# Kernel optimization log

Measured on AMD Instinct MI355X. Metric: run time of the kernel, lower is better.

## Reference

```python
import jax, jax.numpy as jnp
import numpy as np

EMBED_DIM = 1024
NUM_HEADS = 8
HEAD_DIM = EMBED_DIM // NUM_HEADS


def setup_inputs() -> dict:
    key = jax.random.key(0)
    k1, k2, k3, k4, k5 = jax.random.split(key, 5)
    B, N, D = 4, 2048, EMBED_DIM
    scale = 1.0 / np.sqrt(D)
    return {
        "representation": jax.random.normal(k1, (B, N, D), dtype=jnp.float32),
        "W_qkv": jax.random.normal(k2, (D, 3 * D), dtype=jnp.float32) * scale,
        "b_qkv": jnp.zeros((3 * D,), dtype=jnp.float32),
        "W_proj": jax.random.normal(k3, (D, D), dtype=jnp.float32) * scale,
        "b_proj": jnp.zeros((D,), dtype=jnp.float32),
    }


def reference(representation, W_qkv, b_qkv, W_proj, b_proj):
    B, N, D = representation.shape
    H, Hd = NUM_HEADS, HEAD_DIM
    qkv = jnp.einsum("bnd,de->bne", representation, W_qkv) + b_qkv  # [B,N,3D]
    q, k, v = jnp.split(qkv, 3, axis=-1)
    # [B,N,D] -> [B,H,N,Hd]
    split_heads = lambda x: x.reshape(B, N, H, Hd).transpose(0, 2, 1, 3)
    q, k, v = split_heads(q), split_heads(k), split_heads(v)
    dots = jnp.einsum("bhqd,bhkd->bhqk", q, k) * (Hd ** -0.5)  # [B,H,N,N]
    attn = jax.nn.softmax(dots, axis=-1)
    out = jnp.einsum("bhqk,bhkd->bhqd", attn, v)
    out = out.transpose(0, 2, 1, 3).reshape(B, N, D)  # merge heads
    return jnp.einsum("bnd,de->bne", out, W_proj) + b_proj
```

## Files before the change

### kernel.cpp

```cpp
#include <hip/hip_runtime.h>
#include <hip/hip_bf16.h>
#include <cstdint>

typedef unsigned short u16;
typedef __attribute__((ext_vector_type(8))) short short8;
typedef __attribute__((ext_vector_type(4))) float f32x4;
typedef __attribute__((ext_vector_type(4))) unsigned short u16x4;
typedef __attribute__((ext_vector_type(4))) unsigned int u32x4;

#define NSEQ 2048
#define DMODEL 1024
#define NH 8
#define HD 128
#define KDIM 1024
#define QSCALE (0.08838834764831845f * 1.4426950408889634f)

__device__ __forceinline__ u16 f2b(float f) {
  __hip_bfloat16 h = __float2bfloat16(f);
  union { __hip_bfloat16 h; u16 u; } cv; cv.h = h; return cv.u;
}
__device__ __forceinline__ f32x4 zero4() { f32x4 z = {0.f, 0.f, 0.f, 0.f}; return z; }

__device__ __forceinline__ void gload_lds16(const u16* g, u16* l) {
  __builtin_amdgcn_global_load_lds(
      (__attribute__((address_space(1))) void*)g,
      (__attribute__((address_space(3))) void*)l, 16, 0, 0);
}

__device__ __forceinline__ int LK(int r) {
  return (r & 0x23) | ((r & 0x0C) << 1) | ((r & 0x10) >> 2);
}

__global__ void cvt_f32_bf16(const float* __restrict__ in, u16* __restrict__ out) {
  const size_t i = ((size_t)blockIdx.x * 256 + threadIdx.x) * 8;
  f32x4 a = *(const f32x4*)&in[i];
  f32x4 b = *(const f32x4*)&in[i + 4];
  short8 o;
#pragma unroll
  for (int j = 0; j < 4; ++j) { o[j] = (short)f2b(a[j]); o[4 + j] = (short)f2b(b[j]); }
  *(short8*)&out[i] = o;
}

__global__ void transpose_k(const float* __restrict__ in, u16* __restrict__ out,
                            int R, int C) {
  __shared__ u16 tile[32][33];
  const int tx = threadIdx.x, ty = threadIdx.y;
  const int c = blockIdx.x * 32 + tx;
  const int r0 = blockIdx.y * 32;
  for (int i = ty; i < 32; i += 8) tile[i][tx] = f2b(in[(size_t)(r0 + i) * C + c]);
  __syncthreads();
  const int oc = r0 + tx;
  const int c0 = blockIdx.x * 32;
  for (int i = ty; i < 32; i += 8) out[(size_t)(c0 + i) * R + oc] = tile[tx][i];
}

template <int MODE>
__global__ __launch_bounds__(256, 3) void gemm128(
    const u16* __restrict__ A, const u16* __restrict__ Bt,
    const float* __restrict__ bias, u16* __restrict__ o0,
    u16* __restrict__ o1, u16* __restrict__ o2, float* __restrict__ of) {
  __shared__ __align__(16) u16 sA[128 * 64];
  __shared__ __align__(16) u16 sB[128 * 64];

  const int tid = threadIdx.x;
  const int lane = tid & 63;
  const int w = tid >> 6;
  const int quad = lane >> 4, ln = lane & 15;
  const int m0 = blockIdx.y * 128, n0 = blockIdx.x * 128;
  const int wm = (w >> 1) * 64, wn = (w & 1) * 64;

  f32x4 acc[4][4];
#pragma unroll
  for (int i = 0; i < 4; ++i)
#pragma unroll
    for (int j = 0; j < 4; ++j) acc[i][j] = zero4();

  const int cbase = w * 4;
  for (int kb = 0; kb < KDIM / 64; ++kb) {
    __syncthreads();
    const int k0 = kb * 64;
#pragma unroll
    for (int i = 0; i < 4; ++i) {
      int c = (cbase + i) * 64 + lane;
      int r = c >> 3, s = c & 7;
      gload_lds16(A + (size_t)(m0 + r) * KDIM + k0 + s * 8, &sA[(cbase + i) * 512]);
      gload_lds16(Bt + (size_t)(n0 + r) * KDIM + k0 + s * 8, &sB[(cbase + i) * 512]);
    }
    __syncthreads();
#pragma unroll
    for (int ks = 0; ks < 2; ++ks) {
      short8 af[4], bf[4];
      const int kc = ks * 4 + quad;
#pragma unroll
      for (int t = 0; t < 4; ++t) {
        af[t] = *(const short8*)&sA[(wm + t * 16 + ln) * 64 + kc * 8];
        bf[t] = *(const short8*)&sB[(wn + t * 16 + ln) * 64 + kc * 8];
      }
#pragma unroll
      for (int mt = 0; mt < 4; ++mt)
#pragma unroll
        for (int nt = 0; nt < 4; ++nt)
          acc[mt][nt] = __builtin_amdgcn_mfma_f32_16x16x32_bf16(
              af[mt], bf[nt], acc[mt][nt], 0, 0, 0);
    }
  }

  if (MODE == 0) {
    const int which = n0 >> 10;
    const int h = (n0 & 1023) >> 7;
#pragma unroll
    for (int mt = 0; mt < 4; ++mt) {
      const int rbase = m0 + wm + mt * 16 + quad * 4;
      const int b = rbase >> 11;
      const int n = rbase & 2047;
#pragma unroll
      for (int nt = 0; nt < 4; ++nt) {
        const int dcol = wn + nt * 16 + ln;
        const float bv = bias[n0 + dcol];
        if (which == 0) {
          u16* p = o0 + ((size_t)(b * NH + h) * NSEQ + n) * HD + dcol;
#pragma unroll
          for (int rr = 0; rr < 4; ++rr)
            p[(size_t)rr * HD] = f2b((acc[mt][nt][rr] + bv) * QSCALE);
        } else if (which == 1) {
          u16* p = o1 + ((size_t)(b * NH + h) * NSEQ + n) * HD + dcol;
#pragma unroll
          for (int rr = 0; rr < 4; ++rr)
            p[(size_t)rr * HD] = f2b(acc[mt][nt][rr] + bv);
        } else {
          u16x4 pk;
#pragma unroll
          for (int rr = 0; rr < 4; ++rr) pk[rr] = f2b(acc[mt][nt][rr] + bv);
          *(u16x4*)&o2[((size_t)(b * NH + h) * HD + dcol) * NSEQ + n] = pk;
        }
      }
    }
  } else {
#pragma unroll
    for (int mt = 0; mt < 4; ++mt) {
      const int rbase = m0 + wm + mt * 16 + quad * 4;
#pragma unroll
      for (int nt = 0; nt < 4; ++nt) {
        const int col = n0 + wn + nt * 16 + ln;
        const float bv = bias[col];
#pragma unroll
        for (int rr = 0; rr < 4; ++rr)
          of[(size_t)(rbase + rr) * DMODEL + col] = acc[mt][nt][rr] + bv;
      }
    }
  }
}

__global__ __launch_bounds__(256, 2) void attn_fused(
    const u16* __restrict__ Q, const u16* __restrict__ K,
    const u16* __restrict__ Vt, u16* __restrict__ AO) {
  __shared__ __align__(16) u16 sK[2][64 * 128];
  __shared__ __align__(16) u16 sV[2][128 * 64];

  const int tid = threadIdx.x;
  const int w = tid >> 6, lane = tid & 63;
  const int quad = lane >> 4, ln = lane & 15;
  const int bh = blockIdx.y;
  const int q0 = blockIdx.x * 128;

  const u16* Qb = Q + ((size_t)bh * NSEQ + q0) * HD;
  const u16* Kb = K + (size_t)bh * NSEQ * HD;
  const u16* Vb = Vt + (size_t)bh * HD * NSEQ;

  int gk_off[4], gv_off[4];
#pragma unroll
  for (int j = 0; j < 4; ++j) {
    const int c = (w * 4 + j) * 64 + lane;
    const int rk = c >> 4, sk_ = c & 15;
    gk_off[j] = LK(rk) * HD + (sk_ ^ (rk & 7)) * 8;
    const int rv = c >> 3, sv_ = c & 7;
    gv_off[j] = rv * NSEQ + (sv_ ^ (rv & 7)) * 8;
  }

  int kfo[4][4], vfo[2][8];
#pragma unroll
  for (int n = 0; n < 4; ++n)
#pragma unroll
    for (int ks = 0; ks < 4; ++ks)
      kfo[n][ks] = (n * 16 + ln) * 128 + ((((ks << 2) | quad) ^ (ln & 7)) * 8);
#pragma unroll
  for (int ks2 = 0; ks2 < 2; ++ks2)
#pragma unroll
    for (int dt = 0; dt < 8; ++dt)
      vfo[ks2][dt] = (dt * 16 + ln) * 64 + ((((ks2 << 2) | quad) ^ (ln & 7)) * 8);

  short8 qf[2][4];
#pragma unroll
  for (int mt = 0; mt < 2; ++mt)
#pragma unroll
    for (int ks = 0; ks < 4; ++ks)
      qf[mt][ks] = *(const short8*)&Qb[(size_t)(w * 32 + mt * 16 + ln) * HD +
                                       ks * 32 + quad * 8];

  f32x4 o[2][8];
#pragma unroll
  for (int mt = 0; mt < 2; ++mt)
#pragma unroll
    for (int dt = 0; dt < 8; ++dt) o[mt][dt] = zero4();
  float l_part[2] = {0.f, 0.f};

#pragma unroll
  for (int j = 0; j < 4; ++j) {
    gload_lds16(Kb + gk_off[j], &sK[0][(w * 4 + j) * 512]);
    gload_lds16(Vb + gv_off[j], &sV[0][(w * 4 + j) * 512]);
  }

  union PU { u32x4 u; short8 s; };

#pragma unroll 1
  for (int it = 0; it < NSEQ / 128; ++it) {
#pragma unroll
    for (int c2 = 0; c2 < 2; ++c2) {
      __syncthreads();

      const int kvn = it * 128 + c2 * 64 + 64;
      if (kvn < NSEQ) {
#pragma unroll
        for (int j = 0; j < 4; ++j) {
          gload_lds16(Kb + (size_t)kvn * HD + gk_off[j],
                      &sK[c2 ^ 1][(w * 4 + j) * 512]);
          gload_lds16(Vb + kvn + gv_off[j], &sV[c2 ^ 1][(w * 4 + j) * 512]);
        }
      }
      const u16* skr = &sK[c2][0];
      const u16* svr = &sV[c2][0];

      __builtin_amdgcn_s_setprio(1);

      f32x4 sacc[4][2];
      PU ph[2][2];

      auto SM = [&](int m) {
#pragma unroll
        for (int mt = 0; mt < 2; ++mt) {
          float e0 = exp2f(sacc[m][mt][0]);
          float e1 = exp2f(sacc[m][mt][1]);
          float e2 = exp2f(sacc[m][mt][2]);
          float e3 = exp2f(sacc[m][mt][3]);
          l_part[mt] += (e0 + e1) + (e2 + e3);
          unsigned a0 = __float_as_uint(e0) + 0x8000u;
          unsigned a1 = __float_as_uint(e1) + 0x8000u;
          unsigned a2 = __float_as_uint(e2) + 0x8000u;
          unsigned a3 = __float_as_uint(e3) + 0x8000u;
          ph[mt][m >> 1].u[(m & 1) * 2 + 0] = __builtin_amdgcn_perm(a1, a0, 0x07060302);
          ph[mt][m >> 1].u[(m & 1) * 2 + 1] = __builtin_amdgcn_perm(a3, a2, 0x07060302);
        }
      };

#pragma unroll
      for (int n = 0; n < 4; ++n) {
#pragma unroll
        for (int mt = 0; mt < 2; ++mt) sacc[n][mt] = zero4();
#pragma unroll
        for (int ks = 0; ks < 4; ++ks) {
          short8 kf = *(const short8*)&skr[kfo[n][ks]];
          sacc[n][0] = __builtin_amdgcn_mfma_f32_16x16x32_bf16(
              kf, qf[0][ks], sacc[n][0], 0, 0, 0);
          sacc[n][1] = __builtin_amdgcn_mfma_f32_16x16x32_bf16(
              kf, qf[1][ks], sacc[n][1], 0, 0, 0);
        }
        if (n) SM(n - 1);
      }

      {
        short8 pf0 = ph[0][0].s, pf1 = ph[1][0].s;
        short8 vf[8];
#pragma unroll
        for (int dt = 0; dt < 8; ++dt)
          vf[dt] = *(const short8*)&svr[vfo[0][dt]];
#pragma unroll
        for (int dt = 0; dt < 8; ++dt) {
          o[0][dt] = __builtin_amdgcn_mfma_f32_16x16x32_bf16(
              pf0, vf[dt], o[0][dt], 0, 0, 0);
          o[1][dt] = __builtin_amdgcn_mfma_f32_16x16x32_bf16(
              pf1, vf[dt], o[1][dt], 0, 0, 0);
        }
      }
      SM(3);
      {
        short8 pf0 = ph[0][1].s, pf1 = ph[1][1].s;
        short8 vf[8];
#pragma unroll
        for (int dt = 0; dt < 8; ++dt)
          vf[dt] = *(const short8*)&svr[vfo[1][dt]];
#pragma unroll
        for (int dt = 0; dt < 8; ++dt) {
          o[0][dt] = __builtin_amdgcn_mfma_f32_16x16x32_bf16(
              pf0, vf[dt], o[0][dt], 0, 0, 0);
          o[1][dt] = __builtin_amdgcn_mfma_f32_16x16x32_bf16(
              pf1, vf[dt], o[1][dt], 0, 0, 0);
        }
      }
      __builtin_amdgcn_s_setprio(0);
    }
  }

  const int b = bh >> 3, h = bh & 7;
#pragma unroll
  for (int mt = 0; mt < 2; ++mt) {
    float v = l_part[mt];
    v += __shfl_xor(v, 16, 64);
    v += __shfl_xor(v, 32, 64);
    float inv[4];
#pragma unroll
    for (int rr = 0; rr < 4; ++rr)
      inv[rr] = 1.0f / __shfl(v, quad * 4 + rr, 64);
    const int rbase = q0 + w * 32 + mt * 16 + quad * 4;
#pragma unroll
    for (int dt = 0; dt < 8; ++dt) {
      const int d = dt * 16 + ln;
#pragma unroll
      for (int rr = 0; rr < 4; ++rr)
        AO[((size_t)b * NSEQ + rbase + rr) * DMODEL + h * HD + d] =
            f2b(o[mt][dt][rr] * inv[rr]);
    }
  }
}

extern "C" void kernel_launch(void* const* d_in, const int* in_sizes, int n_in,
                              void* d_out, int out_size, void* d_ws, size_t ws_size,
                              hipStream_t stream) {
  const float* X = (const float*)d_in[0];
  const float* Wqkv = (const float*)d_in[1];
  const float* bqkv = (const float*)d_in[2];
  const float* Wproj = (const float*)d_in[3];
  const float* bproj = (const float*)d_in[4];
  float* out = (float*)d_out;

  const size_t NEED_BYTES =
      2ull * (8388608  + 3072 * 1024 + 1024 * 1024 + 3 * 8388608 + 8388608);
  if (ws_size < NEED_BYTES) return;

  u16* ws = (u16*)d_ws;
  u16* Xb = ws;
  u16* WqkvT = Xb + 8388608;
  u16* WprojT = WqkvT + 3072 * 1024;
  u16* Qb = WprojT + 1024 * 1024;
  u16* Kb = Qb + 8388608;
  u16* Vtb = Kb + 8388608;
  u16* AO = Vtb + 8388608;

  cvt_f32_bf16<<<8388608 / (256 * 8), 256, 0, stream>>>(X, Xb);
  transpose_k<<<dim3(3072 / 32, 1024 / 32), dim3(32, 8), 0, stream>>>(Wqkv, WqkvT, 1024, 3072);
  transpose_k<<<dim3(1024 / 32, 1024 / 32), dim3(32, 8), 0, stream>>>(Wproj, WprojT, 1024, 1024);
  gemm128<0><<<dim3(3072 / 128, 8192 / 128), 256, 0, stream>>>(
      Xb, WqkvT, bqkv, Qb, Kb, Vtb, nullptr);
  attn_fused<<<dim3(2048 / 128, 32), 256, 0, stream>>>(Qb, Kb, Vtb, AO);
  gemm128<1><<<dim3(1024 / 128, 8192 / 128), 256, 0, stream>>>(
      AO, WprojT, bproj, nullptr, nullptr, nullptr, out);
}
```

Before: 273.3 us.

## Load V fragments directly from global memory instead of staging in LDS

```diff
diff --git a/kernel.cpp b/kernel.cpp
--- a/kernel.cpp
+++ b/kernel.cpp
@@ -155,7 +155,6 @@
     const u16* __restrict__ Q, const u16* __restrict__ K,
     const u16* __restrict__ Vt, u16* __restrict__ AO) {
   __shared__ __align__(16) u16 sK[2][64 * 128];
-  __shared__ __align__(16) u16 sV[2][128 * 64];
 
   const int tid = threadIdx.x;
   const int w = tid >> 6, lane = tid & 63;
@@ -167,27 +166,22 @@
   const u16* Kb = K + (size_t)bh * NSEQ * HD;
   const u16* Vb = Vt + (size_t)bh * HD * NSEQ;
 
-  int gk_off[4], gv_off[4];
+  int gk_off[4];
 #pragma unroll
   for (int j = 0; j < 4; ++j) {
     const int c = (w * 4 + j) * 64 + lane;
     const int rk = c >> 4, sk_ = c & 15;
     gk_off[j] = LK(rk) * HD + (sk_ ^ (rk & 7)) * 8;
-    const int rv = c >> 3, sv_ = c & 7;
-    gv_off[j] = rv * NSEQ + (sv_ ^ (rv & 7)) * 8;
-  }
-
-  int kfo[4][4], vfo[2][8];
-#pragma unroll
-  for (int n = 0; n < 4; ++n)
-#pragma unroll
-    for (int ks = 0; ks < 4; ++ks)
-      kfo[n][ks] = (n * 16 + ln) * 128 + ((((ks << 2) | quad) ^ (ln & 7)) * 8);
-#pragma unroll
-  for (int ks2 = 0; ks2 < 2; ++ks2)
-#pragma unroll
-    for (int dt = 0; dt < 8; ++dt)
-      vfo[ks2][dt] = (dt * 16 + ln) * 64 + ((((ks2 << 2) | quad) ^ (ln & 7)) * 8);
+  }
+
+  int kbase[4], kslot[4];
+#pragma unroll
+  for (int n = 0; n < 4; ++n) kbase[n] = (n * 16 + ln) * 128;
+#pragma unroll
+  for (int ks = 0; ks < 4; ++ks)
+    kslot[ks] = (((ks << 2) | quad) ^ (ln & 7)) * 8;
+
+  const u16* vbase = Vb + (size_t)ln * NSEQ + quad * 8;
 
   short8 qf[2][4];
 #pragma unroll
@@ -205,10 +199,8 @@
   float l_part[2] = {0.f, 0.f};
 
 #pragma unroll
-  for (int j = 0; j < 4; ++j) {
+  for (int j = 0; j < 4; ++j)
     gload_lds16(Kb + gk_off[j], &sK[0][(w * 4 + j) * 512]);
-    gload_lds16(Vb + gv_off[j], &sV[0][(w * 4 + j) * 512]);
-  }
 
   union PU { u32x4 u; short8 s; };
 
@@ -216,19 +208,25 @@
   for (int it = 0; it < NSEQ / 128; ++it) {
 #pragma unroll
     for (int c2 = 0; c2 < 2; ++c2) {
+      const int kv = it * 128 + c2 * 64;
       __syncthreads();
 
-      const int kvn = it * 128 + c2 * 64 + 64;
+      short8 vf[2][8];
+#pragma unroll
+      for (int dt = 0; dt < 8; ++dt)
+        vf[0][dt] = *(const short8*)&vbase[(size_t)dt * 16 * NSEQ + kv];
+#pragma unroll
+      for (int dt = 0; dt < 8; ++dt)
+        vf[1][dt] = *(const short8*)&vbase[(size_t)dt * 16 * NSEQ + kv + 32];
+
+      const int kvn = kv + 64;
       if (kvn < NSEQ) {
 #pragma unroll
-        for (int j = 0; j < 4; ++j) {
+        for (int j = 0; j < 4; ++j)
           gload_lds16(Kb + (size_t)kvn * HD + gk_off[j],
                       &sK[c2 ^ 1][(w * 4 + j) * 512]);
-          gload_lds16(Vb + kvn + gv_off[j], &sV[c2 ^ 1][(w * 4 + j) * 512]);
-        }
       }
       const u16* skr = &sK[c2][0];
-      const u16* svr = &sV[c2][0];
 
       __builtin_amdgcn_s_setprio(1);
 
@@ -258,7 +256,7 @@
         for (int mt = 0; mt < 2; ++mt) sacc[n][mt] = zero4();
 #pragma unroll
         for (int ks = 0; ks < 4; ++ks) {
-          short8 kf = *(const short8*)&skr[kfo[n][ks]];
+          short8 kf = *(const short8*)&skr[kbase[n] + kslot[ks]];
           sacc[n][0] = __builtin_amdgcn_mfma_f32_16x16x32_bf16(
               kf, qf[0][ks], sacc[n][0], 0, 0, 0);
           sacc[n][1] = __builtin_amdgcn_mfma_f32_16x16x32_bf16(
@@ -269,31 +267,23 @@
 
       {
         short8 pf0 = ph[0][0].s, pf1 = ph[1][0].s;
-        short8 vf[8];
-#pragma unroll
-        for (int dt = 0; dt < 8; ++dt)
-          vf[dt] = *(const short8*)&svr[vfo[0][dt]];
 #pragma unroll
         for (int dt = 0; dt < 8; ++dt) {
           o[0][dt] = __builtin_amdgcn_mfma_f32_16x16x32_bf16(
-              pf0, vf[dt], o[0][dt], 0, 0, 0);
+              pf0, vf[0][dt], o[0][dt], 0, 0, 0);
           o[1][dt] = __builtin_amdgcn_mfma_f32_16x16x32_bf16(
-              pf1, vf[dt], o[1][dt], 0, 0, 0);
+              pf1, vf[0][dt], o[1][dt], 0, 0, 0);
         }
       }
       SM(3);
       {
         short8 pf0 = ph[0][1].s, pf1 = ph[1][1].s;
-        short8 vf[8];
-#pragma unroll
-        for (int dt = 0; dt < 8; ++dt)
-          vf[dt] = *(const short8*)&svr[vfo[1][dt]];
 #pragma unroll
         for (int dt = 0; dt < 8; ++dt) {
           o[0][dt] = __builtin_amdgcn_mfma_f32_16x16x32_bf16(
-              pf0, vf[dt], o[0][dt], 0, 0, 0);
+              pf0, vf[1][dt], o[0][dt], 0, 0, 0);
           o[1][dt] = __builtin_amdgcn_mfma_f32_16x16x32_bf16(
-              pf1, vf[dt], o[1][dt], 0, 0, 0);
+              pf1, vf[1][dt], o[1][dt], 0, 0, 0);
         }
       }
       __builtin_amdgcn_s_setprio(0);
```

Measured after the change: 326.1 us. 1.19x slower.
